# Kernel tuning notes

Measured on AMD Instinct MI355X. Metric: run time of the kernel, lower is better.

Reference implementation:

```python
import jax, jax.numpy as jnp
import numpy as np

FREQ_RES = 100.0 / 256.0
NUM_FILTERS = 6
_CFG = [(0.5, 4.0), (4.0, 8.0), (8.0, 12.0), (12.0, 16.0), (16.0, 24.0), (24.0, 30.0)]
BANDS = [(int(a / FREQ_RES), int(b / FREQ_RES)) for a, b in _CFG]  # (start_bin, end_bin)


def _interp_idx(n_src, n_dst):
    # torch F.interpolate bilinear, align_corners=False, along last dim (T dim is identity since same size)
    j = np.arange(n_dst)
    src = np.maximum((j + 0.5) * n_src / n_dst - 0.5, 0.0)
    x0 = np.floor(src).astype(np.int32)
    x1 = np.minimum(x0 + 1, n_src - 1)
    w = (src - x0).astype(np.float32)
    return x0, x1, w


def _gelu(x):
    return jax.nn.gelu(x, approximate=False)


def _forward(spec, centers, widths, gains, align_w, align_b, fc1_w, fc1_b, fc2_w, fc2_b,
             band_gain, gate_w, gate_b, proj_w, proj_b, bn_gamma, bn_beta, bn_mean, bn_var):
    B, C, T, F = spec.shape
    N = NUM_FILTERS
    band_feats = []
    for i, (s, e) in enumerate(BANDS):
        nb = e - s + 1
        sl = spec[:, :, :, s:e + 1]                       # [B,C,T,nb]
        mu = jax.nn.softplus(centers[i]) + s              # [C,N]
        mu = jnp.clip(mu, s, s + nb - 1)
        std = jnp.clip(jax.nn.softplus(widths[i]) + 1e-3, 0.5, 2.0 * nb / N)
        freqs = jnp.arange(nb, dtype=spec.dtype)          # relative bins [nb]
        g = jnp.exp(-0.5 * ((freqs[None, None, :] - mu[:, :, None]) / std[:, :, None]) ** 2)  # [C,N,nb]
        w = gains[i][:, :, None] * g / (g.sum(-1, keepdims=True) + 1e-6)
        filt = jnp.einsum('bctf,cnf->bctn', sl, w)        # [B,C,T,N]
        aligned = jnp.einsum('bctn,dc->bdtn', filt, align_w[i]) + align_b[i][None, :, None, None]
        band_feats.append(aligned)
    band_stack = jnp.stack(band_feats, axis=1)            # [B,6,C,T,N]
    nb_bands = band_stack.shape[1]
    x = band_stack.reshape(B, nb_bands * C, T, N)
    h = _gelu(jnp.einsum('bktn,ok->botn', x, fc1_w) + fc1_b[None, :, None, None])
    attn = jnp.einsum('botn,ko->bktn', h, fc2_w) + fc2_b[None, :, None, None]
    attn = jax.nn.softmax(attn.reshape(B, nb_bands, C, T, N), axis=1)  # softmax over bands
    band_stack = band_stack * attn * band_gain[None, :, None, None, None]
    enhanced = jnp.zeros_like(spec)
    for i, (s, e) in enumerate(BANDS):
        nb = e - s + 1
        narrow = band_stack[:, i]                         # [B,C,T,N]
        x0, x1, wl = _interp_idx(NUM_FILTERS, nb)
        wl = jnp.asarray(wl, dtype=spec.dtype)
        bf = narrow[..., x0] * (1.0 - wl) + narrow[..., x1] * wl   # [B,C,T,nb]
        enhanced = enhanced.at[:, :, :, s:e + 1].add(bf)
    residual = enhanced - spec
    gate = jax.nn.sigmoid(jnp.einsum('bctf,dc->bdtf', residual, gate_w) + gate_b[None, :, None, None])
    enhanced2 = spec + gate * residual
    y = jnp.einsum('bctf,dc->bdtf', enhanced2, proj_w) + proj_b[None, :, None, None]
    y = (y - bn_mean[None, :, None, None]) / jnp.sqrt(bn_var[None, :, None, None] + 1e-5)
    y = y * bn_gamma[None, :, None, None] + bn_beta[None, :, None, None]
    return _gelu(y)


def setup_inputs() -> dict:
    key = jax.random.key(0)
    ks = jax.random.split(key, 8)
    B, C, T, F, N = 64, 3, 3000, 103, NUM_FILTERS
    spec = jax.random.normal(ks[0], (B, C, T, F), dtype=jnp.float32)
    centers = jnp.stack([jnp.broadcast_to(jnp.linspace(a, b, N, dtype=jnp.float32) / FREQ_RES, (C, N)) for a, b in _CFG])
    widths = jnp.stack([jnp.full((C, N), (b - a) / N / FREQ_RES, dtype=jnp.float32) for a, b in _CFG])
    gains = jnp.ones((6, C, N), jnp.float32)
    align_w = jax.random.normal(ks[1], (6, C, C), dtype=jnp.float32) / np.sqrt(C)
    align_b = jax.random.normal(ks[2], (6, C), dtype=jnp.float32) * 0.02
    inter = 2 * C
    fc1_w = jax.random.normal(ks[3], (inter, 6 * C), dtype=jnp.float32) / np.sqrt(6 * C)
    fc1_b = jnp.zeros((inter,), jnp.float32)
    fc2_w = jax.random.normal(ks[4], (6 * C, inter), dtype=jnp.float32) / np.sqrt(inter)
    fc2_b = jnp.zeros((6 * C,), jnp.float32)
    band_gain = jnp.ones((6,), jnp.float32)
    gate_w = jax.random.normal(ks[5], (C, C), dtype=jnp.float32) / np.sqrt(C)
    gate_b = jnp.zeros((C,), jnp.float32)
    proj_w = jax.random.normal(ks[6], (C, C), dtype=jnp.float32) / np.sqrt(C)
    proj_b = jnp.zeros((C,), jnp.float32)
    bn_gamma = jnp.ones((C,), jnp.float32)
    bn_beta = jnp.zeros((C,), jnp.float32)
    bn_mean = jnp.zeros((C,), jnp.float32)
    bn_var = jnp.ones((C,), jnp.float32)
    return {"spec": spec, "centers": centers, "widths": widths, "gains": gains,
            "align_w": align_w, "align_b": align_b, "fc1_w": fc1_w, "fc1_b": fc1_b,
            "fc2_w": fc2_w, "fc2_b": fc2_b, "band_gain": band_gain,
            "gate_w": gate_w, "gate_b": gate_b, "proj_w": proj_w, "proj_b": proj_b,
            "bn_gamma": bn_gamma, "bn_beta": bn_beta, "bn_mean": bn_mean, "bn_var": bn_var}


def reference(spec, centers, widths, gains, align_w, align_b, fc1_w, fc1_b, fc2_w, fc2_b,
              band_gain, gate_w, gate_b, proj_w, proj_b, bn_gamma, bn_beta, bn_mean, bn_var):
    return _forward(spec, centers, widths, gains, align_w, align_b, fc1_w, fc1_b, fc2_w, fc2_b,
                    band_gain, gate_w, gate_b, proj_w, proj_b, bn_gamma, bn_beta, bn_mean, bn_var)
```

## Files before the change

kernel.cpp:

```cpp
#include <hip/hip_runtime.h>
#include <math.h>

namespace {

constexpr int C_ = 3, T_ = 3000, F_ = 103, NB_ = 6;
constexpr int TT = 20;
constexpr int NT = 3;
constexpr int BS[NB_]  = {1, 10, 20, 30, 40, 61};
constexpr int BNB[NB_] = {10, 11, 11, 11, 22, 16};
constexpr int WSTART[NB_] = {0, 5, 10, 15, 20, 30};
constexpr int WCNT[NB_]   = {6, 6, 6, 6, 11, 9};
constexpr int WOFF[NB_]   = {0, 6, 12, 18, 24, 35};
constexpr int WROW = 44;
constexpr int WTOTU = 18 * WROW;
constexpr int SPW = 39;
constexpr int SPECW = C_ * TT * SPW;
constexpr int ERS = 52;
constexpr int EPL = TT * ERS;
constexpr int POOLU = 3 * EPL;
constexpr int PLANE = T_ * F_;

__device__ __forceinline__ float softplus_(float x) {
  return fmaxf(x, 0.0f) + log1pf(expf(-fabsf(x)));
}
__device__ __forceinline__ float sigmoid_(float z) {
  return 1.0f / (1.0f + __expf(-z));
}
__device__ __forceinline__ float gelu_(float x) {
  return x * sigmoid_(1.595769122f * x * (1.0f + 0.044715f * x * x));
}
__device__ __forceinline__ unsigned bf16_rne_(float x) {
  unsigned b = __float_as_uint(x);
  b += 0x7FFFu + ((b >> 16) & 1u);
  return b >> 16;
}
__device__ __forceinline__ float bl_(unsigned u) { return __uint_as_float(u << 16); }
__device__ __forceinline__ float bh_(unsigned u) { return __uint_as_float(u & 0xffff0000u); }

__global__ __launch_bounds__(128)
void prep_kernel(const float* __restrict__ centers,
                 const float* __restrict__ widths,
                 const float* __restrict__ gains,
                 const float* __restrict__ proj_w,
                 const float* __restrict__ proj_b,
                 const float* __restrict__ bn_gamma,
                 const float* __restrict__ bn_beta,
                 const float* __restrict__ bn_mean,
                 const float* __restrict__ bn_var,
                 float* __restrict__ ws)
{
  unsigned* wsU = (unsigned*)ws;
  const int q = threadIdx.x;
  if (q < 108) {
    int i = q / 18;
    int p = q - i * 18;
    int s = BS[i], nb = BNB[i];
    float mu = softplus_(centers[q]) + (float)s;
    mu = fminf(fmaxf(mu, (float)s), (float)(s + nb - 1));
    float sd = softplus_(widths[q]) + 0.001f;
    sd = fminf(fmaxf(sd, 0.5f), 2.0f * (float)nb / 6.0f);
    float sum = 0.0f;
    for (int f = 0; f < nb; ++f) {
      float d = ((float)f - mu) / sd;
      sum += __expf(-0.5f * d * d);
    }
    float sc = gains[q] / (sum + 1e-6f);
    float wtmp[22];
    for (int f = 0; f < nb; ++f) {
      float d = ((float)f - mu) / sd;
      wtmp[f] = sc * __expf(-0.5f * d * d);
    }
    for (int e = 0; e < WCNT[i]; ++e) {
      int flo = 2 * (WSTART[i] + e) - s;
      int fhi = flo + 1;
      unsigned lo = (flo >= 0 && flo < nb) ? bf16_rne_(wtmp[flo]) : 0u;
      unsigned hi = (fhi >= 0 && fhi < nb) ? bf16_rne_(wtmp[fhi]) : 0u;
      wsU[p * WROW + WOFF[i] + e] = lo | (hi << 16);
    }
  } else if (q < 117) {
    int k = q - 108, d = k / 3;
    float sc = bn_gamma[d] / sqrtf(bn_var[d] + 1e-5f);
    ws[WTOTU + k] = proj_w[k] * sc;
  } else if (q < 120) {
    int d = q - 117;
    float sc = bn_gamma[d] / sqrtf(bn_var[d] + 1e-5f);
    ws[WTOTU + 9 + d] = (proj_b[d] - bn_mean[d]) * sc + bn_beta[d];
  }
}

__global__ __launch_bounds__(256, 6)
void sleepband_kernel(const float* __restrict__ spec,
                      const float* __restrict__ ws,
                      const float* __restrict__ align_w,
                      const float* __restrict__ align_b,
                      const float* __restrict__ fc1_w,
                      const float* __restrict__ fc1_b,
                      const float* __restrict__ fc2_w,
                      const float* __restrict__ fc2_b,
                      const float* __restrict__ band_gain,
                      const float* __restrict__ gate_w,
                      const float* __restrict__ gate_b,
                      float* __restrict__ out)
{
  __shared__ unsigned sPoolU[POOLU];
  __shared__ unsigned sWu[WTOTU];
  __shared__ float sBand[TT][109];
  __shared__ float sAw[54], sAb[18], sF1[108], sF1b[6], sF2[108], sF2b[18],
                   sBg[6], sGw[9], sGb[3], sPw[9], sPb[3];

  const int tid = threadIdx.x;
  const int b   = blockIdx.y;
  const float* specB = spec + (size_t)b * C_ * PLANE;
  float* outBase = out + (size_t)b * C_ * PLANE;
  const unsigned* wsU = (const unsigned*)ws;

  for (int k = tid; k < WTOTU; k += 256) sWu[k] = wsU[k];
  if (tid < 54)  sAw[tid]  = align_w[tid];
  if (tid < 18)  sAb[tid]  = align_b[tid];
  if (tid < 108) sF1[tid]  = fc1_w[tid];
  if (tid < 6)   sF1b[tid] = fc1_b[tid];
  if (tid < 108) sF2[tid]  = fc2_w[tid];
  if (tid < 18)  sF2b[tid] = fc2_b[tid];
  if (tid < 6)   sBg[tid]  = band_gain[tid];
  if (tid < 9)   sGw[tid]  = gate_w[tid];
  if (tid < 3)   sGb[tid]  = gate_b[tid];
  if (tid < 9)   sPw[tid]  = ws[WTOTU + tid];
  if (tid < 3)   sPb[tid]  = ws[WTOTU + 9 + tid];

  for (int tile = 0; tile < NT; ++tile) {
    const int t0 = (blockIdx.x * NT + tile) * TT;

    for (int li = tid; li < SPECW; li += 256) {
      int c   = li / (TT * SPW);
      int rem = li - c * (TT * SPW);
      int tt  = rem / SPW;
      int w   = rem - tt * SPW;
      const float* gr = specB + (size_t)c * PLANE + (size_t)(t0 + tt) * F_;
      unsigned lo = bf16_rne_(gr[2 * w]);
      unsigned hi = bf16_rne_(gr[2 * w + 1]);
      sPoolU[li] = lo | (hi << 16);
    }
    __syncthreads();

    if (tid < 180) {
      const int g  = tid / TT;
      const int tt = tid - g * TT;
      const int c  = g / 3;
      const int np = g - c * 3;
      const int n0 = 2 * np;
      const unsigned* srow = &sPoolU[(c * TT + tt) * SPW];
      const unsigned* w0 = &sWu[(c * 6 + n0) * WROW];
      const unsigned* w1 = w0 + WROW;
      #pragma unroll
      for (int i = 0; i < NB_; ++i) {
        float a0 = 0.0f, a1 = 0.0f;
        #pragma unroll
        for (int e = 0; e < WCNT[i]; ++e) {
          unsigned su = srow[WSTART[i] + e];
          float s0 = bl_(su), s1 = bh_(su);
          unsigned u0 = w0[WOFF[i] + e], u1 = w1[WOFF[i] + e];
          a0 += s0 * bl_(u0); a0 += s1 * bh_(u0);
          a1 += s0 * bl_(u1); a1 += s1 * bh_(u1);
        }
        sBand[tt][(i * 3 + c) * 6 + n0]     = a0;
        sBand[tt][(i * 3 + c) * 6 + n0 + 1] = a1;
      }
    }
    __syncthreads();

    if (tid < 6 * TT) {
      int n  = tid / TT;
      int tt = tid - n * TT;
      float al[18];
      #pragma unroll
      for (int i = 0; i < 6; ++i) {
        float f0 = sBand[tt][(i * 3 + 0) * 6 + n];
        float f1 = sBand[tt][(i * 3 + 1) * 6 + n];
        float f2 = sBand[tt][(i * 3 + 2) * 6 + n];
        #pragma unroll
        for (int d = 0; d < 3; ++d)
          al[i * 3 + d] = sAw[i * 9 + d * 3 + 0] * f0 + sAw[i * 9 + d * 3 + 1] * f1 +
                          sAw[i * 9 + d * 3 + 2] * f2 + sAb[i * 3 + d];
      }
      float h[6];
      #pragma unroll
      for (int o = 0; o < 6; ++o) {
        float acc = sF1b[o];
        #pragma unroll
        for (int k = 0; k < 18; ++k) acc += sF1[o * 18 + k] * al[k];
        h[o] = gelu_(acc);
      }
      float at[18];
      #pragma unroll
      for (int k = 0; k < 18; ++k) {
        float acc = sF2b[k];
        #pragma unroll
        for (int o = 0; o < 6; ++o) acc += sF2[k * 6 + o] * h[o];
        at[k] = acc;
      }
      #pragma unroll
      for (int c = 0; c < 3; ++c) {
        float m = at[c];
        #pragma unroll
        for (int i = 1; i < 6; ++i) m = fmaxf(m, at[i * 3 + c]);
        float e[6], ssum = 0.0f;
        #pragma unroll
        for (int i = 0; i < 6; ++i) { e[i] = __expf(at[i * 3 + c] - m); ssum += e[i]; }
        float inv = 1.0f / ssum;
        #pragma unroll
        for (int i = 0; i < 6; ++i)
          sBand[tt][(i * 3 + c) * 6 + n] = al[i * 3 + c] * (e[i] * inv) * sBg[i];
      }
    }
    __syncthreads();

    if (tid < C_ * TT) {
      const int c  = tid / TT;
      const int tt = tid - c * TT;
      float bnd[36];
      #pragma unroll
      for (int i = 0; i < 6; ++i)
        #pragma unroll
        for (int n = 0; n < 6; ++n)
          bnd[i * 6 + n] = sBand[tt][(i * 3 + c) * 6 + n];
      unsigned* rowU = &sPoolU[c * EPL + tt * ERS];
      float pend = 0.0f;
      float carry = 0.0f;
      #pragma unroll
      for (int i = 0; i < NB_; ++i) {
        #pragma unroll
        for (int j = 0; j < BNB[i]; ++j) {
          const int f = BS[i] + j;
          float src = ((float)j + 0.5f) * 6.0f / (float)BNB[i] - 0.5f;
          src = src > 0.0f ? src : 0.0f;
          int   x0 = (int)src;
          int   x1 = (x0 < 5) ? x0 + 1 : 5;
          float wl = src - (float)x0;
          float v  = bnd[i * 6 + x0] * (1.0f - wl) + bnd[i * 6 + x1] * wl;
          if (j == 0) v += carry;
          if (i < NB_ - 1 && j == BNB[i] - 1) {
            carry = v;
          } else {
            if (f & 1) rowU[f >> 1] = bf16_rne_(pend) | (bf16_rne_(v) << 16);
            else       pend = v;
          }
        }
      }
      rowU[38] = bf16_rne_(pend);
      #pragma unroll
      for (int w = 39; w < ERS; ++w) rowU[w] = 0u;
    }
    __syncthreads();

    float gw[9], pw[9], gb3[3], pb3[3];
    #pragma unroll
    for (int k = 0; k < 9; ++k) { gw[k] = sGw[k]; pw[k] = sPw[k]; }
    #pragma unroll
    for (int k = 0; k < 3; ++k) { gb3[k] = sGb[k]; pb3[k] = sPb[k]; }

    const float* sp0 = specB + (size_t)t0 * F_;
    float* outB = outBase + (size_t)t0 * F_;
    for (int e4 = tid; e4 < (TT * F_) / 4; e4 += 256) {
      const int e = e4 * 4;
      const float4 sA = *(const float4*)(sp0 + e);
      const float4 sB = *(const float4*)(sp0 + PLANE + e);
      const float4 sC = *(const float4*)(sp0 + 2 * PLANE + e);
      float4 oA, oB, oC;
      const float* sAp = (const float*)&sA; const float* sBp = (const float*)&sB;
      const float* sCp = (const float*)&sC;
      float* oAp = (float*)&oA; float* oBp = (float*)&oB; float* oCp = (float*)&oC;
      #pragma unroll
      for (int j = 0; j < 4; ++j) {
        const int idx = e + j;
        const int tt  = idx / F_;
        const int f   = idx - tt * F_;
        const int wd  = tt * ERS + (f >> 1);
        const unsigned ua = sPoolU[0 * EPL + wd];
        const unsigned ub = sPoolU[1 * EPL + wd];
        const unsigned uc = sPoolU[2 * EPL + wd];
        const bool hi = (f & 1);
        float e0 = hi ? bh_(ua) : bl_(ua);
        float e1 = hi ? bh_(ub) : bl_(ub);
        float e2 = hi ? bh_(uc) : bl_(uc);
        float sv0 = sAp[j], sv1 = sBp[j], sv2 = sCp[j];
        float r0 = e0 - sv0, r1 = e1 - sv1, r2 = e2 - sv2;
        float e20 = sv0 + sigmoid_(gw[0] * r0 + gw[1] * r1 + gw[2] * r2 + gb3[0]) * r0;
        float e21 = sv1 + sigmoid_(gw[3] * r0 + gw[4] * r1 + gw[5] * r2 + gb3[1]) * r1;
        float e22 = sv2 + sigmoid_(gw[6] * r0 + gw[7] * r1 + gw[8] * r2 + gb3[2]) * r2;
        float y0 = pw[0] * e20 + pw[1] * e21 + pw[2] * e22 + pb3[0];
        float y1 = pw[3] * e20 + pw[4] * e21 + pw[5] * e22 + pb3[1];
        float y2 = pw[6] * e20 + pw[7] * e21 + pw[8] * e22 + pb3[2];
        oAp[j] = gelu_(y0); oBp[j] = gelu_(y1); oCp[j] = gelu_(y2);
      }
      *(float4*)(outB + e) = oA;
      *(float4*)(outB + PLANE + e) = oB;
      *(float4*)(outB + 2 * PLANE + e) = oC;
    }
    __syncthreads();
  }
}

}

extern "C" void kernel_launch(void* const* d_in, const int* in_sizes, int n_in,
                              void* d_out, int out_size, void* d_ws, size_t ws_size,
                              hipStream_t stream) {
  (void)n_in; (void)out_size; (void)ws_size;
  const int B = in_sizes[0] / (C_ * T_ * F_);
  float* ws = (float*)d_ws;
  prep_kernel<<<1, 128, 0, stream>>>(
      (const float*)d_in[1],  (const float*)d_in[2],  (const float*)d_in[3],
      (const float*)d_in[13], (const float*)d_in[14], (const float*)d_in[15],
      (const float*)d_in[16], (const float*)d_in[17], (const float*)d_in[18], ws);
  dim3 grid(T_ / (TT * NT), B);
  sleepband_kernel<<<grid, 256, 0, stream>>>(
      (const float*)d_in[0],  ws,
      (const float*)d_in[4],  (const float*)d_in[5],
      (const float*)d_in[6],  (const float*)d_in[7],  (const float*)d_in[8],
      (const float*)d_in[9],  (const float*)d_in[10], (const float*)d_in[11],
      (const float*)d_in[12], (float*)d_out);
}
```

Before: 234.8 us.

## Split tile into per-wavefront sub-tiles and replace block barriers with wave fences

```diff
diff --git a/kernel.cpp b/kernel.cpp
--- a/kernel.cpp
+++ b/kernel.cpp
@@ -6,6 +6,7 @@
 constexpr int C_ = 3, T_ = 3000, F_ = 103, NB_ = 6;
 constexpr int TT = 20;
 constexpr int NT = 3;
+constexpr int RPW = 5;
 constexpr int BS[NB_]  = {1, 10, 20, 30, 40, 61};
 constexpr int BNB[NB_] = {10, 11, 11, 11, 22, 16};
 constexpr int WSTART[NB_] = {0, 5, 10, 15, 20, 30};
@@ -13,12 +14,9 @@
 constexpr int WOFF[NB_]   = {0, 6, 12, 18, 24, 35};
 constexpr int WROW = 44;
 constexpr int WTOTU = 18 * WROW;
-constexpr int SPW = 39;
-constexpr int SPECW = C_ * TT * SPW;
-constexpr int ERS = 52;
-constexpr int EPL = TT * ERS;
-constexpr int POOLU = 3 * EPL;
+constexpr int SREG = 780;
 constexpr int PLANE = T_ * F_;
+constexpr int WELE = RPW * F_;
 
 __device__ __forceinline__ float softplus_(float x) {
   return fmaxf(x, 0.0f) + log1pf(expf(-fabsf(x)));
@@ -36,6 +34,10 @@
 }
 __device__ __forceinline__ float bl_(unsigned u) { return __uint_as_float(u << 16); }
 __device__ __forceinline__ float bh_(unsigned u) { return __uint_as_float(u & 0xffff0000u); }
+__device__ __forceinline__ void wfence_() {
+  asm volatile("s_waitcnt lgkmcnt(0)" ::: "memory");
+  __builtin_amdgcn_wave_barrier();
+}
 
 __global__ __launch_bounds__(128)
 void prep_kernel(const float* __restrict__ centers,
@@ -102,17 +104,20 @@
                       const float* __restrict__ gate_b,
                       float* __restrict__ out)
 {
-  __shared__ unsigned sPoolU[POOLU];
+  __shared__ unsigned sW4[4][SREG];
   __shared__ unsigned sWu[WTOTU];
   __shared__ float sBand[TT][109];
   __shared__ float sAw[54], sAb[18], sF1[108], sF1b[6], sF2[108], sF2b[18],
                    sBg[6], sGw[9], sGb[3], sPw[9], sPb[3];
 
-  const int tid = threadIdx.x;
-  const int b   = blockIdx.y;
+  const int tid  = threadIdx.x;
+  const int w    = tid >> 6;
+  const int lane = tid & 63;
+  const int b    = blockIdx.y;
   const float* specB = spec + (size_t)b * C_ * PLANE;
   float* outBase = out + (size_t)b * C_ * PLANE;
   const unsigned* wsU = (const unsigned*)ws;
+  unsigned* reg = &sW4[w][0];
 
   for (int k = tid; k < WTOTU; k += 256) sWu[k] = wsU[k];
   if (tid < 54)  sAw[tid]  = align_w[tid];
@@ -126,29 +131,40 @@
   if (tid < 3)   sGb[tid]  = gate_b[tid];
   if (tid < 9)   sPw[tid]  = ws[WTOTU + tid];
   if (tid < 3)   sPb[tid]  = ws[WTOTU + 9 + tid];
+  __syncthreads();
+
+  float gw[9], pw[9], gb3[3], pb3[3];
+  #pragma unroll
+  for (int k = 0; k < 9; ++k) { gw[k] = sGw[k]; pw[k] = sPw[k]; }
+  #pragma unroll
+  for (int k = 0; k < 3; ++k) { gb3[k] = sGb[k]; pb3[k] = sPb[k]; }
 
   for (int tile = 0; tile < NT; ++tile) {
     const int t0 = (blockIdx.x * NT + tile) * TT;
-
-    for (int li = tid; li < SPECW; li += 256) {
-      int c   = li / (TT * SPW);
-      int rem = li - c * (TT * SPW);
-      int tt  = rem / SPW;
-      int w   = rem - tt * SPW;
-      const float* gr = specB + (size_t)c * PLANE + (size_t)(t0 + tt) * F_;
-      unsigned lo = bf16_rne_(gr[2 * w]);
-      unsigned hi = bf16_rne_(gr[2 * w + 1]);
-      sPoolU[li] = lo | (hi << 16);
-    }
-    __syncthreads();
-
-    if (tid < 180) {
-      const int g  = tid / TT;
-      const int tt = tid - g * TT;
-      const int c  = g / 3;
-      const int np = g - c * 3;
-      const int n0 = 2 * np;
-      const unsigned* srow = &sPoolU[(c * TT + tt) * SPW];
+    const int tw = t0 + w * RPW;
+
+    for (int li = lane; li < RPW * C_ * 40; li += 64) {
+      int ttl = li / 120;
+      int rem = li - ttl * 120;
+      int c   = rem / 40;
+      int wd  = rem - c * 40;
+      unsigned v = 0u;
+      if (wd < 39) {
+        const float* gr = specB + (size_t)c * PLANE + (size_t)(tw + ttl) * F_;
+        v = bf16_rne_(gr[2 * wd]) | (bf16_rne_(gr[2 * wd + 1]) << 16);
+      }
+      reg[li] = v;
+    }
+    wfence_();
+
+    if (lane < 45) {
+      const int g   = lane / RPW;
+      const int ttl = lane - g * RPW;
+      const int c   = g / 3;
+      const int np  = g - c * 3;
+      const int n0  = 2 * np;
+      const int row = w * RPW + ttl;
+      const unsigned* srow = reg + (ttl * 3 + c) * 40;
       const unsigned* w0 = &sWu[(c * 6 + n0) * WROW];
       const unsigned* w1 = w0 + WROW;
       #pragma unroll
@@ -162,21 +178,22 @@
           a0 += s0 * bl_(u0); a0 += s1 * bh_(u0);
           a1 += s0 * bl_(u1); a1 += s1 * bh_(u1);
         }
-        sBand[tt][(i * 3 + c) * 6 + n0]     = a0;
-        sBand[tt][(i * 3 + c) * 6 + n0 + 1] = a1;
-      }
-    }
-    __syncthreads();
-
-    if (tid < 6 * TT) {
-      int n  = tid / TT;
-      int tt = tid - n * TT;
+        sBand[row][(i * 3 + c) * 6 + n0]     = a0;
+        sBand[row][(i * 3 + c) * 6 + n0 + 1] = a1;
+      }
+    }
+    wfence_();
+
+    if (lane < 6 * RPW) {
+      const int n   = lane / RPW;
+      const int ttl = lane - n * RPW;
+      const int row = w * RPW + ttl;
       float al[18];
       #pragma unroll
       for (int i = 0; i < 6; ++i) {
-        float f0 = sBand[tt][(i * 3 + 0) * 6 + n];
-        float f1 = sBand[tt][(i * 3 + 1) * 6 + n];
-        float f2 = sBand[tt][(i * 3 + 2) * 6 + n];
+        float f0 = sBand[row][(i * 3 + 0) * 6 + n];
+        float f1 = sBand[row][(i * 3 + 1) * 6 + n];
+        float f2 = sBand[row][(i * 3 + 2) * 6 + n];
         #pragma unroll
         for (int d = 0; d < 3; ++d)
           al[i * 3 + d] = sAw[i * 9 + d * 3 + 0] * f0 + sAw[i * 9 + d * 3 + 1] * f1 +
@@ -209,21 +226,22 @@
         float inv = 1.0f / ssum;
         #pragma unroll
         for (int i = 0; i < 6; ++i)
-          sBand[tt][(i * 3 + c) * 6 + n] = al[i * 3 + c] * (e[i] * inv) * sBg[i];
-      }
-    }
-    __syncthreads();
-
-    if (tid < C_ * TT) {
-      const int c  = tid / TT;
-      const int tt = tid - c * TT;
+          sBand[row][(i * 3 + c) * 6 + n] = al[i * 3 + c] * (e[i] * inv) * sBg[i];
+      }
+    }
+    wfence_();
+
+    if (lane < C_ * RPW) {
+      const int c   = lane / RPW;
+      const int ttl = lane - c * RPW;
+      const int row = w * RPW + ttl;
       float bnd[36];
       #pragma unroll
       for (int i = 0; i < 6; ++i)
         #pragma unroll
         for (int n = 0; n < 6; ++n)
-          bnd[i * 6 + n] = sBand[tt][(i * 3 + c) * 6 + n];
-      unsigned* rowU = &sPoolU[c * EPL + tt * ERS];
+          bnd[i * 6 + n] = sBand[row][(i * 3 + c) * 6 + n];
+      unsigned* rowU = reg + c * (RPW * 52) + ttl * 52;
       float pend = 0.0f;
       float carry = 0.0f;
       #pragma unroll
@@ -248,20 +266,41 @@
       }
       rowU[38] = bf16_rne_(pend);
       #pragma unroll
-      for (int w = 39; w < ERS; ++w) rowU[w] = 0u;
-    }
-    __syncthreads();
-
-    float gw[9], pw[9], gb3[3], pb3[3];
-    #pragma unroll
-    for (int k = 0; k < 9; ++k) { gw[k] = sGw[k]; pw[k] = sPw[k]; }
-    #pragma unroll
-    for (int k = 0; k < 3; ++k) { gb3[k] = sGb[k]; pb3[k] = sPb[k]; }
+      for (int wdz = 39; wdz < 52; ++wdz) rowU[wdz] = 0u;
+    }
+    wfence_();
 
     const float* sp0 = specB + (size_t)t0 * F_;
     float* outB = outBase + (size_t)t0 * F_;
-    for (int e4 = tid; e4 < (TT * F_) / 4; e4 += 256) {
-      const int e = e4 * 4;
+    const int wbeg = WELE * w, wend = wbeg + WELE;
+    const int astart = (wbeg + 3) & ~3, aend = wend & ~3;
+
+    auto finElem = [&](int idx) {
+      const int tt  = idx / F_;
+      const int f   = idx - tt * F_;
+      const int ttl = tt - w * RPW;
+      const int wd  = ttl * 52 + (f >> 1);
+      const bool hi = (f & 1);
+      const unsigned ua = reg[wd];
+      const unsigned ub = reg[260 + wd];
+      const unsigned uc = reg[520 + wd];
+      float e0 = hi ? bh_(ua) : bl_(ua);
+      float e1 = hi ? bh_(ub) : bl_(ub);
+      float e2 = hi ? bh_(uc) : bl_(uc);
+      float sv0 = sp0[idx], sv1 = sp0[PLANE + idx], sv2 = sp0[2 * PLANE + idx];
+      float r0 = e0 - sv0, r1 = e1 - sv1, r2 = e2 - sv2;
+      float e20 = sv0 + sigmoid_(gw[0] * r0 + gw[1] * r1 + gw[2] * r2 + gb3[0]) * r0;
+      float e21 = sv1 + sigmoid_(gw[3] * r0 + gw[4] * r1 + gw[5] * r2 + gb3[1]) * r1;
+      float e22 = sv2 + sigmoid_(gw[6] * r0 + gw[7] * r1 + gw[8] * r2 + gb3[2]) * r2;
+      outB[idx] = gelu_(pw[0] * e20 + pw[1] * e21 + pw[2] * e22 + pb3[0]);
+      outB[PLANE + idx] = gelu_(pw[3] * e20 + pw[4] * e21 + pw[5] * e22 + pb3[1]);
+      outB[2 * PLANE + idx] = gelu_(pw[6] * e20 + pw[7] * e21 + pw[8] * e22 + pb3[2]);
+    };
+
+    if (lane < astart - wbeg) finElem(wbeg + lane);
+    if (lane < wend - aend)   finElem(aend + lane);
+
+    for (int e = astart + 4 * lane; e < aend; e += 256) {
       const float4 sA = *(const float4*)(sp0 + e);
       const float4 sB = *(const float4*)(sp0 + PLANE + e);
       const float4 sC = *(const float4*)(sp0 + 2 * PLANE + e);
@@ -274,11 +313,12 @@
         const int idx = e + j;
         const int tt  = idx / F_;
         const int f   = idx - tt * F_;
-        const int wd  = tt * ERS + (f >> 1);
-        const unsigned ua = sPoolU[0 * EPL + wd];
-        const unsigned ub = sPoolU[1 * EPL + wd];
-        const unsigned uc = sPoolU[2 * EPL + wd];
+        const int ttl = tt - w * RPW;
+        const int wd  = ttl * 52 + (f >> 1);
         const bool hi = (f & 1);
+        const unsigned ua = reg[wd];
+        const unsigned ub = reg[260 + wd];
+        const unsigned uc = reg[520 + wd];
         float e0 = hi ? bh_(ua) : bl_(ua);
         float e1 = hi ? bh_(ub) : bl_(ub);
         float e2 = hi ? bh_(uc) : bl_(uc);
@@ -287,16 +327,15 @@
         float e20 = sv0 + sigmoid_(gw[0] * r0 + gw[1] * r1 + gw[2] * r2 + gb3[0]) * r0;
         float e21 = sv1 + sigmoid_(gw[3] * r0 + gw[4] * r1 + gw[5] * r2 + gb3[1]) * r1;
         float e22 = sv2 + sigmoid_(gw[6] * r0 + gw[7] * r1 + gw[8] * r2 + gb3[2]) * r2;
-        float y0 = pw[0] * e20 + pw[1] * e21 + pw[2] * e22 + pb3[0];
-        float y1 = pw[3] * e20 + pw[4] * e21 + pw[5] * e22 + pb3[1];
-        float y2 = pw[6] * e20 + pw[7] * e21 + pw[8] * e22 + pb3[2];
-        oAp[j] = gelu_(y0); oBp[j] = gelu_(y1); oCp[j] = gelu_(y2);
+        oAp[j] = gelu_(pw[0] * e20 + pw[1] * e21 + pw[2] * e22 + pb3[0]);
+        oBp[j] = gelu_(pw[3] * e20 + pw[4] * e21 + pw[5] * e22 + pb3[1]);
+        oCp[j] = gelu_(pw[6] * e20 + pw[7] * e21 + pw[8] * e22 + pb3[2]);
       }
       *(float4*)(outB + e) = oA;
       *(float4*)(outB + PLANE + e) = oB;
       *(float4*)(outB + 2 * PLANE + e) = oC;
     }
-    __syncthreads();
+    wfence_();
   }
 }
 
```

Result: slower. 356.6 us (+51.9%).

## Split fused kernel into band-stats and output kernels via workspace band buffer

Applied to the files above, without the earlier changes.

```diff
diff --git a/kernel.cpp b/kernel.cpp
--- a/kernel.cpp
+++ b/kernel.cpp
@@ -4,21 +4,24 @@
 namespace {
 
 constexpr int C_ = 3, T_ = 3000, F_ = 103, NB_ = 6;
-constexpr int TT = 20;
-constexpr int NT = 3;
 constexpr int BS[NB_]  = {1, 10, 20, 30, 40, 61};
 constexpr int BNB[NB_] = {10, 11, 11, 11, 22, 16};
 constexpr int WSTART[NB_] = {0, 5, 10, 15, 20, 30};
 constexpr int WCNT[NB_]   = {6, 6, 6, 6, 11, 9};
 constexpr int WOFF[NB_]   = {0, 6, 12, 18, 24, 35};
-constexpr int WROW = 44;
+constexpr int WROW  = 44;
 constexpr int WTOTU = 18 * WROW;
-constexpr int SPW = 39;
-constexpr int SPECW = C_ * TT * SPW;
-constexpr int ERS = 52;
-constexpr int EPL = TT * ERS;
-constexpr int POOLU = 3 * EPL;
+constexpr int TAPOFF  = 804;
+constexpr int BANDOFF = 2048;
+constexpr int BROW = 54;
 constexpr int PLANE = T_ * F_;
+constexpr int TT1 = 32;
+constexpr int SROWP = 121;
+constexpr int BROWP = 55;
+constexpr int TT2 = 20;
+constexpr int TTF = 20, NTF = 3;
+constexpr int SPW = 39, SPECW = C_ * TTF * SPW, ERS = 52, EPL = TTF * ERS,
+              POOLU = 3 * EPL;
 
 __device__ __forceinline__ float softplus_(float x) {
   return fmaxf(x, 0.0f) + log1pf(expf(-fabsf(x)));
@@ -36,8 +39,11 @@
 }
 __device__ __forceinline__ float bl_(unsigned u) { return __uint_as_float(u << 16); }
 __device__ __forceinline__ float bh_(unsigned u) { return __uint_as_float(u & 0xffff0000u); }
-
-__global__ __launch_bounds__(128)
+__device__ __forceinline__ float b16_(unsigned short u) {
+  return __uint_as_float((unsigned)u << 16);
+}
+
+__global__ __launch_bounds__(256)
 void prep_kernel(const float* __restrict__ centers,
                  const float* __restrict__ widths,
                  const float* __restrict__ gains,
@@ -85,26 +91,252 @@
     int d = q - 117;
     float sc = bn_gamma[d] / sqrtf(bn_var[d] + 1e-5f);
     ws[WTOTU + 9 + d] = (proj_b[d] - bn_mean[d]) * sc + bn_beta[d];
+  } else if (q >= 128 && q < 128 + F_) {
+    const int f = q - 128;
+    unsigned cols = 0;
+    float w4[4] = {0.f, 0.f, 0.f, 0.f};
+    int slot = 0;
+    #pragma unroll
+    for (int i = 0; i < NB_; ++i) {
+      if (f >= BS[i] && f < BS[i] + BNB[i]) {
+        int j = f - BS[i];
+        float src = ((float)j + 0.5f) * 6.0f / (float)BNB[i] - 0.5f;
+        src = src > 0.0f ? src : 0.0f;
+        int x0 = (int)src;
+        int x1 = (x0 < 5) ? x0 + 1 : 5;
+        float wl = src - (float)x0;
+        cols |= ((unsigned)(i * 18 + x0) << (16 * slot))
+              | ((unsigned)(i * 18 + x1) << (16 * slot + 8));
+        w4[2 * slot] = 1.0f - wl;
+        w4[2 * slot + 1] = wl;
+        ++slot;
+      }
+    }
+    wsU[TAPOFF + f * 5] = cols;
+    #pragma unroll
+    for (int k = 0; k < 4; ++k) ws[TAPOFF + f * 5 + 1 + k] = w4[k];
+  }
+}
+
+__global__ __launch_bounds__(192)
+void band_kernel(const float* __restrict__ spec,
+                 const float* __restrict__ ws,
+                 const float* __restrict__ align_w,
+                 const float* __restrict__ align_b,
+                 const float* __restrict__ fc1_w,
+                 const float* __restrict__ fc1_b,
+                 const float* __restrict__ fc2_w,
+                 const float* __restrict__ fc2_b,
+                 const float* __restrict__ band_gain,
+                 unsigned* __restrict__ band)
+{
+  __shared__ unsigned specP[TT1 * SROWP];
+  __shared__ unsigned bandL[TT1 * BROWP];
+  __shared__ unsigned sWu[WTOTU];
+  __shared__ float sAw[54], sAb[18], sF1[108], sF1b[6], sF2[108], sF2b[18], sBg[6];
+
+  const int tid = threadIdx.x;
+  const int b   = blockIdx.y;
+  const int t0  = blockIdx.x * TT1;
+  const float* specB = spec + (size_t)b * C_ * PLANE;
+  const unsigned* wsU = (const unsigned*)ws;
+
+  for (int k = tid; k < WTOTU; k += 192) sWu[k] = wsU[k];
+  if (tid < 54)  sAw[tid]  = align_w[tid];
+  if (tid < 18)  sAb[tid]  = align_b[tid];
+  if (tid < 108) sF1[tid]  = fc1_w[tid];
+  if (tid < 6)   sF1b[tid] = fc1_b[tid];
+  if (tid < 108) sF2[tid]  = fc2_w[tid];
+  if (tid < 18)  sF2b[tid] = fc2_b[tid];
+  if (tid < 6)   sBg[tid]  = band_gain[tid];
+
+  for (int li = tid; li < TT1 * 120; li += 192) {
+    int tt  = li / 120;
+    int rem = li - tt * 120;
+    int c   = rem / 40;
+    int wd  = rem - c * 40;
+    unsigned v = 0u;
+    if (wd < 39 && t0 + tt < T_) {
+      const float* gr = specB + (size_t)c * PLANE + (size_t)(t0 + tt) * F_;
+      v = bf16_rne_(gr[2 * wd]) | (bf16_rne_(gr[2 * wd + 1]) << 16);
+    }
+    specP[tt * SROWP + c * 40 + wd] = v;
+  }
+  __syncthreads();
+
+  {
+    const int tt = tid / 6;
+    const int n  = tid - tt * 6;
+    if (t0 + tt < T_) {
+      float filt[NB_][3];
+      #pragma unroll
+      for (int i = 0; i < NB_; ++i) {
+        #pragma unroll
+        for (int c = 0; c < 3; ++c) {
+          const unsigned* srow = &specP[tt * SROWP + c * 40];
+          const unsigned* wr = &sWu[(c * 6 + n) * WROW];
+          float a = 0.0f;
+          #pragma unroll
+          for (int e = 0; e < WCNT[i]; ++e) {
+            unsigned su = srow[WSTART[i] + e];
+            unsigned wu = wr[WOFF[i] + e];
+            a += bl_(su) * bl_(wu);
+            a += bh_(su) * bh_(wu);
+          }
+          filt[i][c] = a;
+        }
+      }
+      float al[18];
+      #pragma unroll
+      for (int i = 0; i < 6; ++i)
+        #pragma unroll
+        for (int d = 0; d < 3; ++d)
+          al[i * 3 + d] = sAw[i * 9 + d * 3 + 0] * filt[i][0] +
+                          sAw[i * 9 + d * 3 + 1] * filt[i][1] +
+                          sAw[i * 9 + d * 3 + 2] * filt[i][2] + sAb[i * 3 + d];
+      float h[6];
+      #pragma unroll
+      for (int o = 0; o < 6; ++o) {
+        float acc = sF1b[o];
+        #pragma unroll
+        for (int k = 0; k < 18; ++k) acc += sF1[o * 18 + k] * al[k];
+        h[o] = gelu_(acc);
+      }
+      unsigned short* bu = (unsigned short*)bandL;
+      #pragma unroll
+      for (int c = 0; c < 3; ++c) {
+        float a[6];
+        #pragma unroll
+        for (int i = 0; i < 6; ++i) {
+          float x = sF2b[i * 3 + c];
+          #pragma unroll
+          for (int o = 0; o < 6; ++o) x += sF2[(i * 3 + c) * 6 + o] * h[o];
+          a[i] = x;
+        }
+        float m = a[0];
+        #pragma unroll
+        for (int i = 1; i < 6; ++i) m = fmaxf(m, a[i]);
+        float e[6], ssum = 0.0f;
+        #pragma unroll
+        for (int i = 0; i < 6; ++i) { e[i] = __expf(a[i] - m); ssum += e[i]; }
+        float inv = 1.0f / ssum;
+        #pragma unroll
+        for (int i = 0; i < 6; ++i) {
+          float v = al[i * 3 + c] * (e[i] * inv) * sBg[i];
+          bu[tt * (2 * BROWP) + i * 18 + c * 6 + n] = (unsigned short)bf16_rne_(v);
+        }
+      }
+    }
+  }
+  __syncthreads();
+
+  for (int li = tid; li < TT1 * BROW; li += 192) {
+    int tt = li / BROW;
+    int wd = li - tt * BROW;
+    if (t0 + tt < T_)
+      band[((size_t)b * T_ + (t0 + tt)) * BROW + wd] = bandL[tt * BROWP + wd];
+  }
+}
+
+__global__ __launch_bounds__(256)
+void out_kernel(const float* __restrict__ spec,
+                const float* __restrict__ ws,
+                const unsigned* __restrict__ band,
+                const float* __restrict__ gate_w,
+                const float* __restrict__ gate_b,
+                float* __restrict__ out)
+{
+  __shared__ unsigned bandL[TT2 * BROWP];
+  __shared__ unsigned sTap[F_ * 5];
+  __shared__ float sGw[9], sGb[3], sPw[9], sPb[3];
+
+  const int tid = threadIdx.x;
+  const int b   = blockIdx.y;
+  const int t0  = blockIdx.x * TT2;
+  const unsigned* wsU = (const unsigned*)ws;
+
+  for (int li = tid; li < TT2 * BROW; li += 256) {
+    int tt = li / BROW;
+    int wd = li - tt * BROW;
+    bandL[tt * BROWP + wd] = band[((size_t)b * T_ + (t0 + tt)) * BROW + wd];
+  }
+  for (int k = tid; k < F_ * 5; k += 256) sTap[k] = wsU[TAPOFF + k];
+  if (tid < 9) sGw[tid] = gate_w[tid];
+  if (tid < 3) sGb[tid] = gate_b[tid];
+  if (tid < 9) sPw[tid] = ws[WTOTU + tid];
+  if (tid < 3) sPb[tid] = ws[WTOTU + 9 + tid];
+  __syncthreads();
+
+  float gw[9], pw[9], gb3[3], pb3[3];
+  #pragma unroll
+  for (int k = 0; k < 9; ++k) { gw[k] = sGw[k]; pw[k] = sPw[k]; }
+  #pragma unroll
+  for (int k = 0; k < 3; ++k) { gb3[k] = sGb[k]; pb3[k] = sPb[k]; }
+
+  const unsigned short* bu = (const unsigned short*)bandL;
+  const float* sp0 = spec + (size_t)b * C_ * PLANE + (size_t)t0 * F_;
+  float* outB = out + (size_t)b * C_ * PLANE + (size_t)t0 * F_;
+
+  for (int e4 = tid; e4 < (TT2 * F_) / 4; e4 += 256) {
+    const int e = e4 * 4;
+    const float4 sA = *(const float4*)(sp0 + e);
+    const float4 sB = *(const float4*)(sp0 + PLANE + e);
+    const float4 sC = *(const float4*)(sp0 + 2 * PLANE + e);
+    float4 oA, oB, oC;
+    const float* sAp = (const float*)&sA; const float* sBp = (const float*)&sB;
+    const float* sCp = (const float*)&sC;
+    float* oAp = (float*)&oA; float* oBp = (float*)&oB; float* oCp = (float*)&oC;
+    #pragma unroll
+    for (int j = 0; j < 4; ++j) {
+      const int idx = e + j;
+      const int tt  = idx / F_;
+      const int f   = idx - tt * F_;
+      const unsigned cp = sTap[f * 5];
+      const float wa0 = __uint_as_float(sTap[f * 5 + 1]);
+      const float wb0 = __uint_as_float(sTap[f * 5 + 2]);
+      const float wa1 = __uint_as_float(sTap[f * 5 + 3]);
+      const float wb1 = __uint_as_float(sTap[f * 5 + 4]);
+      const int base = tt * (2 * BROWP);
+      const int ca0 = cp & 0xffu, cb0 = (cp >> 8) & 0xffu;
+      const int ca1 = (cp >> 16) & 0xffu, cb1 = cp >> 24;
+      float e0 = wa0 * b16_(bu[base + ca0])      + wb0 * b16_(bu[base + cb0])
+               + wa1 * b16_(bu[base + ca1])      + wb1 * b16_(bu[base + cb1]);
+      float e1 = wa0 * b16_(bu[base + ca0 + 6])  + wb0 * b16_(bu[base + cb0 + 6])
+               + wa1 * b16_(bu[base + ca1 + 6])  + wb1 * b16_(bu[base + cb1 + 6]);
+      float e2 = wa0 * b16_(bu[base + ca0 + 12]) + wb0 * b16_(bu[base + cb0 + 12])
+               + wa1 * b16_(bu[base + ca1 + 12]) + wb1 * b16_(bu[base + cb1 + 12]);
+      float sv0 = sAp[j], sv1 = sBp[j], sv2 = sCp[j];
+      float r0 = e0 - sv0, r1 = e1 - sv1, r2 = e2 - sv2;
+      float e20 = sv0 + sigmoid_(gw[0] * r0 + gw[1] * r1 + gw[2] * r2 + gb3[0]) * r0;
+      float e21 = sv1 + sigmoid_(gw[3] * r0 + gw[4] * r1 + gw[5] * r2 + gb3[1]) * r1;
+      float e22 = sv2 + sigmoid_(gw[6] * r0 + gw[7] * r1 + gw[8] * r2 + gb3[2]) * r2;
+      oAp[j] = gelu_(pw[0] * e20 + pw[1] * e21 + pw[2] * e22 + pb3[0]);
+      oBp[j] = gelu_(pw[3] * e20 + pw[4] * e21 + pw[5] * e22 + pb3[1]);
+      oCp[j] = gelu_(pw[6] * e20 + pw[7] * e21 + pw[8] * e22 + pb3[2]);
+    }
+    *(float4*)(outB + e) = oA;
+    *(float4*)(outB + PLANE + e) = oB;
+    *(float4*)(outB + 2 * PLANE + e) = oC;
   }
 }
 
 __global__ __launch_bounds__(256, 6)
-void sleepband_kernel(const float* __restrict__ spec,
-                      const float* __restrict__ ws,
-                      const float* __restrict__ align_w,
-                      const float* __restrict__ align_b,
-                      const float* __restrict__ fc1_w,
-                      const float* __restrict__ fc1_b,
-                      const float* __restrict__ fc2_w,
-                      const float* __restrict__ fc2_b,
-                      const float* __restrict__ band_gain,
-                      const float* __restrict__ gate_w,
-                      const float* __restrict__ gate_b,
-                      float* __restrict__ out)
+void fused_kernel(const float* __restrict__ spec,
+                  const float* __restrict__ ws,
+                  const float* __restrict__ align_w,
+                  const float* __restrict__ align_b,
+                  const float* __restrict__ fc1_w,
+                  const float* __restrict__ fc1_b,
+                  const float* __restrict__ fc2_w,
+                  const float* __restrict__ fc2_b,
+                  const float* __restrict__ band_gain,
+                  const float* __restrict__ gate_w,
+                  const float* __restrict__ gate_b,
+                  float* __restrict__ out)
 {
   __shared__ unsigned sPoolU[POOLU];
   __shared__ unsigned sWu[WTOTU];
-  __shared__ float sBand[TT][109];
+  __shared__ float sBand[TTF][109];
   __shared__ float sAw[54], sAb[18], sF1[108], sF1b[6], sF2[108], sF2b[18],
                    sBg[6], sGw[9], sGb[3], sPw[9], sPb[3];
 
@@ -127,28 +359,24 @@
   if (tid < 9)   sPw[tid]  = ws[WTOTU + tid];
   if (tid < 3)   sPb[tid]  = ws[WTOTU + 9 + tid];
 
-  for (int tile = 0; tile < NT; ++tile) {
-    const int t0 = (blockIdx.x * NT + tile) * TT;
-
+  for (int tile = 0; tile < NTF; ++tile) {
+    const int t0 = (blockIdx.x * NTF + tile) * TTF;
     for (int li = tid; li < SPECW; li += 256) {
-      int c   = li / (TT * SPW);
-      int rem = li - c * (TT * SPW);
+      int c   = li / (TTF * SPW);
+      int rem = li - c * (TTF * SPW);
       int tt  = rem / SPW;
       int w   = rem - tt * SPW;
       const float* gr = specB + (size_t)c * PLANE + (size_t)(t0 + tt) * F_;
-      unsigned lo = bf16_rne_(gr[2 * w]);
-      unsigned hi = bf16_rne_(gr[2 * w + 1]);
-      sPoolU[li] = lo | (hi << 16);
+      sPoolU[li] = bf16_rne_(gr[2 * w]) | (bf16_rne_(gr[2 * w + 1]) << 16);
     }
     __syncthreads();
-
     if (tid < 180) {
-      const int g  = tid / TT;
-      const int tt = tid - g * TT;
+      const int g  = tid / TTF;
+      const int tt = tid - g * TTF;
       const int c  = g / 3;
       const int np = g - c * 3;
       const int n0 = 2 * np;
-      const unsigned* srow = &sPoolU[(c * TT + tt) * SPW];
+      const unsigned* srow = &sPoolU[(c * TTF + tt) * SPW];
       const unsigned* w0 = &sWu[(c * 6 + n0) * WROW];
       const unsigned* w1 = w0 + WROW;
       #pragma unroll
@@ -167,10 +395,9 @@
       }
     }
     __syncthreads();
-
-    if (tid < 6 * TT) {
-      int n  = tid / TT;
-      int tt = tid - n * TT;
+    if (tid < 6 * TTF) {
+      int n  = tid / TTF;
+      int tt = tid - n * TTF;
       float al[18];
       #pragma unroll
       for (int i = 0; i < 6; ++i) {
@@ -213,10 +440,9 @@
       }
     }
     __syncthreads();
-
-    if (tid < C_ * TT) {
-      const int c  = tid / TT;
-      const int tt = tid - c * TT;
+    if (tid < C_ * TTF) {
+      const int c  = tid / TTF;
+      const int tt = tid - c * TTF;
       float bnd[36];
       #pragma unroll
       for (int i = 0; i < 6; ++i)
@@ -224,8 +450,7 @@
         for (int n = 0; n < 6; ++n)
           bnd[i * 6 + n] = sBand[tt][(i * 3 + c) * 6 + n];
       unsigned* rowU = &sPoolU[c * EPL + tt * ERS];
-      float pend = 0.0f;
-      float carry = 0.0f;
+      float pend = 0.0f, carry = 0.0f;
       #pragma unroll
       for (int i = 0; i < NB_; ++i) {
         #pragma unroll
@@ -238,9 +463,8 @@
           float wl = src - (float)x0;
           float v  = bnd[i * 6 + x0] * (1.0f - wl) + bnd[i * 6 + x1] * wl;
           if (j == 0) v += carry;
-          if (i < NB_ - 1 && j == BNB[i] - 1) {
-            carry = v;
-          } else {
+          if (i < NB_ - 1 && j == BNB[i] - 1) carry = v;
+          else {
             if (f & 1) rowU[f >> 1] = bf16_rne_(pend) | (bf16_rne_(v) << 16);
             else       pend = v;
           }
@@ -251,16 +475,14 @@
       for (int w = 39; w < ERS; ++w) rowU[w] = 0u;
     }
     __syncthreads();
-
     float gw[9], pw[9], gb3[3], pb3[3];
     #pragma unroll
     for (int k = 0; k < 9; ++k) { gw[k] = sGw[k]; pw[k] = sPw[k]; }
     #pragma unroll
     for (int k = 0; k < 3; ++k) { gb3[k] = sGb[k]; pb3[k] = sPb[k]; }
-
     const float* sp0 = specB + (size_t)t0 * F_;
     float* outB = outBase + (size_t)t0 * F_;
-    for (int e4 = tid; e4 < (TT * F_) / 4; e4 += 256) {
+    for (int e4 = tid; e4 < (TTF * F_) / 4; e4 += 256) {
       const int e = e4 * 4;
       const float4 sA = *(const float4*)(sp0 + e);
       const float4 sB = *(const float4*)(sp0 + PLANE + e);
@@ -287,10 +509,9 @@
         float e20 = sv0 + sigmoid_(gw[0] * r0 + gw[1] * r1 + gw[2] * r2 + gb3[0]) * r0;
         float e21 = sv1 + sigmoid_(gw[3] * r0 + gw[4] * r1 + gw[5] * r2 + gb3[1]) * r1;
         float e22 = sv2 + sigmoid_(gw[6] * r0 + gw[7] * r1 + gw[8] * r2 + gb3[2]) * r2;
-        float y0 = pw[0] * e20 + pw[1] * e21 + pw[2] * e22 + pb3[0];
-        float y1 = pw[3] * e20 + pw[4] * e21 + pw[5] * e22 + pb3[1];
-        float y2 = pw[6] * e20 + pw[7] * e21 + pw[8] * e22 + pb3[2];
-        oAp[j] = gelu_(y0); oBp[j] = gelu_(y1); oCp[j] = gelu_(y2);
+        oAp[j] = gelu_(pw[0] * e20 + pw[1] * e21 + pw[2] * e22 + pb3[0]);
+        oBp[j] = gelu_(pw[3] * e20 + pw[4] * e21 + pw[5] * e22 + pb3[1]);
+        oCp[j] = gelu_(pw[6] * e20 + pw[7] * e21 + pw[8] * e22 + pb3[2]);
       }
       *(float4*)(outB + e) = oA;
       *(float4*)(outB + PLANE + e) = oB;
@@ -305,18 +526,34 @@
 extern "C" void kernel_launch(void* const* d_in, const int* in_sizes, int n_in,
                               void* d_out, int out_size, void* d_ws, size_t ws_size,
                               hipStream_t stream) {
-  (void)n_in; (void)out_size; (void)ws_size;
+  (void)n_in; (void)out_size;
   const int B = in_sizes[0] / (C_ * T_ * F_);
   float* ws = (float*)d_ws;
-  prep_kernel<<<1, 128, 0, stream>>>(
+  prep_kernel<<<1, 256, 0, stream>>>(
       (const float*)d_in[1],  (const float*)d_in[2],  (const float*)d_in[3],
       (const float*)d_in[13], (const float*)d_in[14], (const float*)d_in[15],
       (const float*)d_in[16], (const float*)d_in[17], (const float*)d_in[18], ws);
-  dim3 grid(T_ / (TT * NT), B);
-  sleepband_kernel<<<grid, 256, 0, stream>>>(
-      (const float*)d_in[0],  ws,
-      (const float*)d_in[4],  (const float*)d_in[5],
-      (const float*)d_in[6],  (const float*)d_in[7],  (const float*)d_in[8],
-      (const float*)d_in[9],  (const float*)d_in[10], (const float*)d_in[11],
-      (const float*)d_in[12], (float*)d_out);
-}
+
+  const size_t needed = ((size_t)BANDOFF + (size_t)B * T_ * BROW) * 4;
+  if (ws_size >= needed) {
+    unsigned* band = (unsigned*)ws + BANDOFF;
+    dim3 g1((T_ + TT1 - 1) / TT1, B);
+    band_kernel<<<g1, 192, 0, stream>>>(
+        (const float*)d_in[0], ws,
+        (const float*)d_in[4], (const float*)d_in[5],
+        (const float*)d_in[6], (const float*)d_in[7], (const float*)d_in[8],
+        (const float*)d_in[9], (const float*)d_in[10], band);
+    dim3 g2(T_ / TT2, B);
+    out_kernel<<<g2, 256, 0, stream>>>(
+        (const float*)d_in[0], ws, band,
+        (const float*)d_in[11], (const float*)d_in[12], (float*)d_out);
+  } else {
+    dim3 gf(T_ / (TTF * NTF), B);
+    fused_kernel<<<gf, 256, 0, stream>>>(
+        (const float*)d_in[0], ws,
+        (const float*)d_in[4],  (const float*)d_in[5],
+        (const float*)d_in[6],  (const float*)d_in[7],  (const float*)d_in[8],
+        (const float*)d_in[9],  (const float*)d_in[10], (const float*)d_in[11],
+        (const float*)d_in[12], (float*)d_out);
+  }
+}
```

New measurement: 285.3 us. 1.22x slower.
